# Kernel tuning notes

Measured on AMD Instinct MI355X. Metric: run time of the kernel, lower is better.

The kernel has to match this reference:

```python
import jax, jax.numpy as jnp
import numpy as np

EPS = 0.001
CTX = 8
POWERS = 2.0 ** jnp.arange(CTX - 1, -1, -1, dtype=jnp.float32)  # [2^7,...,1]


def _normalize_rows(x):
    return x / jnp.linalg.norm(x, axis=1, keepdims=True)


def _layer(side, inp, normal, offset, W, bias):
    # inp: None for first layer, else previous layer output
    if inp is None:
        inp = jnp.concatenate([bias, jax.nn.sigmoid(jnp.clip(side, EPS, 1.0 - EPS))])
    else:
        inp = jnp.concatenate([bias, inp])
    bits = (side @ normal > offset).astype(jnp.float32)          # [CTX]
    gating = jnp.dot(bits, POWERS).astype(jnp.int32)              # scalar context index
    logit_in = jnp.log(inp) - jnp.log1p(-inp)                     # torch.logit
    out = jax.nn.sigmoid(logit_in @ W[gating])                    # gather slice + GEMV
    return jnp.clip(out, EPS, 1.0 - EPS)


def setup_inputs() -> dict:
    key = jax.random.key(0)
    ks = jax.random.split(key, 10)
    input_dim, dims = 1024, [1024, 1024, 512, 1]  # [in] + layer_dims + [out]
    side_info = jax.random.normal(ks[0], (input_dim,), dtype=jnp.float32)
    d = {"side_info": side_info}
    for i, (p, c) in enumerate(zip(dims[:-1], dims[1:])):
        d[f"W{i}"] = jnp.full((2 ** CTX, p + 1, c), 1.0 / (p + 1), dtype=jnp.float32)
        d[f"N{i}"] = _normalize_rows(jax.random.normal(ks[1 + i], (input_dim, CTX), dtype=jnp.float32))
        d[f"O{i}"] = jax.random.normal(ks[4 + i], (CTX,), dtype=jnp.float32)
        d[f"B{i}"] = EPS + jax.random.uniform(ks[7 + i], (1,), dtype=jnp.float32) * (1.0 - 2.0 * EPS)
    return d


def reference(side_info, W0, W1, W2, N0, N1, N2, O0, O1, O2, B0, B1, B2):
    side = side_info.astype(jnp.float32)
    out = None
    for W, N, O, B in ((W0, N0, O0, B0), (W1, N1, O1, B1), (W2, N2, O2, B2)):
        out = _layer(side, out, N, O, W, B)
    return out
```

## Files before the change

### kernel.cpp

```cpp
#include <hip/hip_runtime.h>
#include <math.h>

#define GLN_EPS 0.001f

__device__ __forceinline__ float clipf_(float v) {
    return fminf(fmaxf(v, GLN_EPS), 1.0f - GLN_EPS);
}
__device__ __forceinline__ float logitf_(float p) {
    return logf(p) - log1pf(-p);
}
__device__ __forceinline__ float sigclip_logit(float z) {
    float s = 1.0f / (1.0f + expf(-z));
    s = clipf_(s);
    return logf(s) - log1pf(-s);
}


__global__ __launch_bounds__(256) void gln_prep(
    const float* __restrict__ side,
    const float* __restrict__ N0, const float* __restrict__ O0,
    const float* __restrict__ N1, const float* __restrict__ O1,
    const float* __restrict__ N2, const float* __restrict__ O2,
    float* __restrict__ ws)
{
    const int bid = blockIdx.x, tid = threadIdx.x;
    if (bid == 0) {
        for (int i = tid; i < 1536; i += 256) ws[i] = 0.0f;
        return;
    }
    const float* __restrict__ N = (bid == 1) ? N0 : (bid == 2) ? N1 : N2;
    const float* __restrict__ O = (bid == 1) ? O0 : (bid == 2) ? O1 : O2;

    float p[8];
#pragma unroll
    for (int k = 0; k < 8; ++k) p[k] = 0.0f;

    for (int i = tid; i < 1024; i += 256) {
        const float s = side[i];
        const float4* n4 = reinterpret_cast<const float4*>(N + (size_t)i * 8);
        const float4 a = n4[0];
        const float4 b = n4[1];
        p[0] += s * a.x; p[1] += s * a.y; p[2] += s * a.z; p[3] += s * a.w;
        p[4] += s * b.x; p[5] += s * b.y; p[6] += s * b.z; p[7] += s * b.w;
    }

    __shared__ float red[4][8];
    const int lane = tid & 63, wid = tid >> 6;
#pragma unroll
    for (int k = 0; k < 8; ++k) {
        float v = p[k];
#pragma unroll
        for (int off = 32; off > 0; off >>= 1) v += __shfl_down(v, off);
        if (lane == 0) red[wid][k] = v;
    }
    __syncthreads();
    if (tid == 0) {
        int g = 0;
#pragma unroll
        for (int k = 0; k < 8; ++k) {
            const float d = red[0][k] + red[1][k] + red[2][k] + red[3][k];
            if (d > O[k]) g |= 1 << (7 - k);
        }
        reinterpret_cast<int*>(ws)[1536 + (bid - 1)] = g;
    }
}

__global__ __launch_bounds__(256) void gln_gemv0(
    const float* __restrict__ side,
    const float* __restrict__ W0,
    const float* __restrict__ B0,
    float* __restrict__ ws)
{
    const int g = reinterpret_cast<const int*>(ws)[1536];
    const float lb = logitf_(B0[0]);
    const size_t base = (size_t)g * 1025u * 1024u;
    const int col = threadIdx.x * 4;

    float4 acc = make_float4(0.f, 0.f, 0.f, 0.f);
    for (int i = blockIdx.x; i < 1025; i += gridDim.x) {
        const float xi = (i == 0) ? lb : clipf_(side[i - 1]);
        const float4 w = *reinterpret_cast<const float4*>(W0 + base + (size_t)i * 1024u + col);
        acc.x += xi * w.x; acc.y += xi * w.y; acc.z += xi * w.z; acc.w += xi * w.w;
    }
    atomicAdd(&ws[col + 0], acc.x);
    atomicAdd(&ws[col + 1], acc.y);
    atomicAdd(&ws[col + 2], acc.z);
    atomicAdd(&ws[col + 3], acc.w);
}

__global__ __launch_bounds__(256) void gln_gemv1(
    const float* __restrict__ W1,
    const float* __restrict__ B1,
    float* __restrict__ ws)
{
    const int g = reinterpret_cast<const int*>(ws)[1537];
    const float lb = logitf_(B1[0]);
    const size_t base = (size_t)g * 1025u * 512u;
    const int col = threadIdx.x * 2;

    float2 acc = make_float2(0.f, 0.f);
    for (int i = blockIdx.x; i < 1025; i += gridDim.x) {
        const float xi = (i == 0) ? lb : sigclip_logit(ws[i - 1]);
        const float2 w = *reinterpret_cast<const float2*>(W1 + base + (size_t)i * 512u + col);
        acc.x += xi * w.x; acc.y += xi * w.y;
    }
    atomicAdd(&ws[1024 + col + 0], acc.x);
    atomicAdd(&ws[1024 + col + 1], acc.y);
}

__global__ __launch_bounds__(256) void gln_final(
    const float* __restrict__ W2,
    const float* __restrict__ B2,
    float* __restrict__ ws,
    float* __restrict__ out)
{
    const int g = reinterpret_cast<const int*>(ws)[1538];
    const size_t base = (size_t)g * 513u;
    const int tid = threadIdx.x;

    float partial = 0.0f;
    for (int i = tid; i < 513; i += 256) {
        const float xi = (i == 0) ? logitf_(B2[0]) : sigclip_logit(ws[1024 + i - 1]);
        partial += xi * W2[base + i];
    }

    __shared__ float red[4];
#pragma unroll
    for (int off = 32; off > 0; off >>= 1) partial += __shfl_down(partial, off);
    if ((tid & 63) == 0) red[tid >> 6] = partial;
    __syncthreads();
    if (tid == 0) {
        const float z = red[0] + red[1] + red[2] + red[3];
        float o = 1.0f / (1.0f + expf(-z));
        out[0] = clipf_(o);
    }
}

extern "C" void kernel_launch(void* const* d_in, const int* in_sizes, int n_in,
                              void* d_out, int out_size, void* d_ws, size_t ws_size,
                              hipStream_t stream) {
    const float* side = (const float*)d_in[0];
    const float* W0   = (const float*)d_in[1];
    const float* N0   = (const float*)d_in[2];
    const float* O0   = (const float*)d_in[3];
    const float* B0   = (const float*)d_in[4];
    const float* W1   = (const float*)d_in[5];
    const float* N1   = (const float*)d_in[6];
    const float* O1   = (const float*)d_in[7];
    const float* B1   = (const float*)d_in[8];
    const float* W2   = (const float*)d_in[9];
    const float* N2   = (const float*)d_in[10];
    const float* O2   = (const float*)d_in[11];
    const float* B2   = (const float*)d_in[12];
    float* out = (float*)d_out;
    float* ws  = (float*)d_ws;

    hipLaunchKernelGGL(gln_prep,  dim3(4),  dim3(256), 0, stream,
                       side, N0, O0, N1, O1, N2, O2, ws);
    hipLaunchKernelGGL(gln_gemv0, dim3(64), dim3(256), 0, stream, side, W0, B0, ws);
    hipLaunchKernelGGL(gln_gemv1, dim3(64), dim3(256), 0, stream, W1, B1, ws);
    hipLaunchKernelGGL(gln_final, dim3(1),  dim3(256), 0, stream, W2, B2, ws, out);
}
```

Before: 1.433 ms.

## Fuse all GLN stages into one cooperative kernel with grid syncs

Replaces four separate launches with one cooperative kernel of 256 blocks that uses grid-wide syncs between the gating, layer-0 GEMV, layer-1 GEMV and final dot-product stages. The GEMVs are re-tiled so each block covers a 64-column chunk and a strided set of rows, reducing partials in shared memory before one atomic per column. The layer-1 GEMV now uses float4 loads instead of float2. The aim is to remove launch gaps and to spread the 4 MB selected weight slice over many more blocks, since the old 64-block grid left much of the GPU idle. The cost is grid-sync overhead, and the cooperative launch requires all 256 blocks to be co-resident.

```diff
diff --git a/kernel.cpp b/kernel.cpp
--- a/kernel.cpp
+++ b/kernel.cpp
@@ -1,7 +1,11 @@
 #include <hip/hip_runtime.h>
+#include <hip/hip_cooperative_groups.h>
 #include <math.h>
 
+namespace cg = cooperative_groups;
+
 #define GLN_EPS 0.001f
+#define NBLK 256
 
 __device__ __forceinline__ float clipf_(float v) {
     return fminf(fmaxf(v, GLN_EPS), 1.0f - GLN_EPS);
@@ -15,149 +19,148 @@
     return logf(s) - log1pf(-s);
 }
 
+struct GlnArgs {
+    const float *side, *W0, *N0, *O0, *B0;
+    const float *W1, *N1, *O1, *B1;
+    const float *W2, *N2, *O2, *B2;
+    float* ws;
+    float* out;
+};
 
-__global__ __launch_bounds__(256) void gln_prep(
-    const float* __restrict__ side,
-    const float* __restrict__ N0, const float* __restrict__ O0,
-    const float* __restrict__ N1, const float* __restrict__ O1,
-    const float* __restrict__ N2, const float* __restrict__ O2,
-    float* __restrict__ ws)
+
+__global__ __launch_bounds__(256) void gln_fused(GlnArgs a)
 {
+    __shared__ float sred[16 * 64];
+    __shared__ float red8[4][8];
+
     const int bid = blockIdx.x, tid = threadIdx.x;
-    if (bid == 0) {
-        for (int i = tid; i < 1536; i += 256) ws[i] = 0.0f;
-        return;
-    }
-    const float* __restrict__ N = (bid == 1) ? N0 : (bid == 2) ? N1 : N2;
-    const float* __restrict__ O = (bid == 1) ? O0 : (bid == 2) ? O1 : O2;
+    float* ws = a.ws;
 
-    float p[8];
+    if (bid < 3) {
+        const float* __restrict__ N = (bid == 0) ? a.N0 : (bid == 1) ? a.N1 : a.N2;
+        const float* __restrict__ O = (bid == 0) ? a.O0 : (bid == 1) ? a.O1 : a.O2;
+        float p[8];
 #pragma unroll
-    for (int k = 0; k < 8; ++k) p[k] = 0.0f;
-
-    for (int i = tid; i < 1024; i += 256) {
-        const float s = side[i];
-        const float4* n4 = reinterpret_cast<const float4*>(N + (size_t)i * 8);
-        const float4 a = n4[0];
-        const float4 b = n4[1];
-        p[0] += s * a.x; p[1] += s * a.y; p[2] += s * a.z; p[3] += s * a.w;
-        p[4] += s * b.x; p[5] += s * b.y; p[6] += s * b.z; p[7] += s * b.w;
-    }
-
-    __shared__ float red[4][8];
-    const int lane = tid & 63, wid = tid >> 6;
-#pragma unroll
-    for (int k = 0; k < 8; ++k) {
-        float v = p[k];
-#pragma unroll
-        for (int off = 32; off > 0; off >>= 1) v += __shfl_down(v, off);
-        if (lane == 0) red[wid][k] = v;
-    }
-    __syncthreads();
-    if (tid == 0) {
-        int g = 0;
+        for (int k = 0; k < 8; ++k) p[k] = 0.0f;
+        for (int i = tid; i < 1024; i += 256) {
+            const float s = a.side[i];
+            const float4* n4 = reinterpret_cast<const float4*>(N + (size_t)i * 8);
+            const float4 u = n4[0], v = n4[1];
+            p[0] += s * u.x; p[1] += s * u.y; p[2] += s * u.z; p[3] += s * u.w;
+            p[4] += s * v.x; p[5] += s * v.y; p[6] += s * v.z; p[7] += s * v.w;
+        }
+        const int lane = tid & 63, wid = tid >> 6;
 #pragma unroll
         for (int k = 0; k < 8; ++k) {
-            const float d = red[0][k] + red[1][k] + red[2][k] + red[3][k];
-            if (d > O[k]) g |= 1 << (7 - k);
+            float v = p[k];
+#pragma unroll
+            for (int off = 32; off > 0; off >>= 1) v += __shfl_down(v, off);
+            if (lane == 0) red8[wid][k] = v;
         }
-        reinterpret_cast<int*>(ws)[1536 + (bid - 1)] = g;
+        __syncthreads();
+        if (tid == 0) {
+            int g = 0;
+#pragma unroll
+            for (int k = 0; k < 8; ++k) {
+                const float d = red8[0][k] + red8[1][k] + red8[2][k] + red8[3][k];
+                if (d > O[k]) g |= 1 << (7 - k);
+            }
+            reinterpret_cast<int*>(ws)[1536 + bid] = g;
+        }
+    } else if (bid == 3) {
+        for (int i = tid; i < 1536; i += 256) ws[i] = 0.0f;
     }
-}
+    cg::this_grid().sync();
 
-__global__ __launch_bounds__(256) void gln_gemv0(
-    const float* __restrict__ side,
-    const float* __restrict__ W0,
-    const float* __restrict__ B0,
-    float* __restrict__ ws)
-{
-    const int g = reinterpret_cast<const int*>(ws)[1536];
-    const float lb = logitf_(B0[0]);
-    const size_t base = (size_t)g * 1025u * 1024u;
-    const int col = threadIdx.x * 4;
+    {
+        const int g0 = reinterpret_cast<const int*>(ws)[1536];
+        const float lb = logitf_(a.B0[0]);
+        const size_t base = (size_t)g0 * (1025u * 1024u);
+        const int colchunk = bid & 15;
+        const int c16 = tid & 15, r16 = tid >> 4;
+        const int rowid = ((bid >> 4) << 4) | r16;
+        const int col = colchunk * 64 + c16 * 4;
 
-    float4 acc = make_float4(0.f, 0.f, 0.f, 0.f);
-    for (int i = blockIdx.x; i < 1025; i += gridDim.x) {
-        const float xi = (i == 0) ? lb : clipf_(side[i - 1]);
-        const float4 w = *reinterpret_cast<const float4*>(W0 + base + (size_t)i * 1024u + col);
-        acc.x += xi * w.x; acc.y += xi * w.y; acc.z += xi * w.z; acc.w += xi * w.w;
+        float4 acc = make_float4(0.f, 0.f, 0.f, 0.f);
+        for (int i = rowid; i < 1025; i += 256) {
+            const float xi = (i == 0) ? lb : clipf_(a.side[i - 1]);
+            const float4 w = *reinterpret_cast<const float4*>(a.W0 + base + (size_t)i * 1024u + col);
+            acc.x += xi * w.x; acc.y += xi * w.y; acc.z += xi * w.z; acc.w += xi * w.w;
+        }
+        *reinterpret_cast<float4*>(&sred[r16 * 64 + c16 * 4]) = acc;
+        __syncthreads();
+        if (tid < 64) {
+            float s = 0.0f;
+#pragma unroll
+            for (int r = 0; r < 16; ++r) s += sred[r * 64 + tid];
+            atomicAdd(&ws[colchunk * 64 + tid], s);
+        }
     }
-    atomicAdd(&ws[col + 0], acc.x);
-    atomicAdd(&ws[col + 1], acc.y);
-    atomicAdd(&ws[col + 2], acc.z);
-    atomicAdd(&ws[col + 3], acc.w);
-}
+    cg::this_grid().sync();
 
-__global__ __launch_bounds__(256) void gln_gemv1(
-    const float* __restrict__ W1,
-    const float* __restrict__ B1,
-    float* __restrict__ ws)
-{
-    const int g = reinterpret_cast<const int*>(ws)[1537];
-    const float lb = logitf_(B1[0]);
-    const size_t base = (size_t)g * 1025u * 512u;
-    const int col = threadIdx.x * 2;
+    {
+        const int g1 = reinterpret_cast<const int*>(ws)[1537];
+        const float lb = logitf_(a.B1[0]);
+        const size_t base = (size_t)g1 * (1025u * 512u);
+        const int colchunk = bid & 7;
+        const int c16 = tid & 15, r16 = tid >> 4;
+        const int rowid = ((bid >> 3) << 4) | r16;
+        const int col = colchunk * 64 + c16 * 4;
 
-    float2 acc = make_float2(0.f, 0.f);
-    for (int i = blockIdx.x; i < 1025; i += gridDim.x) {
-        const float xi = (i == 0) ? lb : sigclip_logit(ws[i - 1]);
-        const float2 w = *reinterpret_cast<const float2*>(W1 + base + (size_t)i * 512u + col);
-        acc.x += xi * w.x; acc.y += xi * w.y;
+        float4 acc = make_float4(0.f, 0.f, 0.f, 0.f);
+        for (int i = rowid; i < 1025; i += 512) {
+            const float xi = (i == 0) ? lb : sigclip_logit(ws[i - 1]);
+            const float4 w = *reinterpret_cast<const float4*>(a.W1 + base + (size_t)i * 512u + col);
+            acc.x += xi * w.x; acc.y += xi * w.y; acc.z += xi * w.z; acc.w += xi * w.w;
+        }
+        __syncthreads();
+        *reinterpret_cast<float4*>(&sred[r16 * 64 + c16 * 4]) = acc;
+        __syncthreads();
+        if (tid < 64) {
+            float s = 0.0f;
+#pragma unroll
+            for (int r = 0; r < 16; ++r) s += sred[r * 64 + tid];
+            atomicAdd(&ws[1024 + colchunk * 64 + tid], s);
+        }
     }
-    atomicAdd(&ws[1024 + col + 0], acc.x);
-    atomicAdd(&ws[1024 + col + 1], acc.y);
-}
+    cg::this_grid().sync();
 
-__global__ __launch_bounds__(256) void gln_final(
-    const float* __restrict__ W2,
-    const float* __restrict__ B2,
-    float* __restrict__ ws,
-    float* __restrict__ out)
-{
-    const int g = reinterpret_cast<const int*>(ws)[1538];
-    const size_t base = (size_t)g * 513u;
-    const int tid = threadIdx.x;
-
-    float partial = 0.0f;
-    for (int i = tid; i < 513; i += 256) {
-        const float xi = (i == 0) ? logitf_(B2[0]) : sigclip_logit(ws[1024 + i - 1]);
-        partial += xi * W2[base + i];
-    }
-
-    __shared__ float red[4];
+    if (bid == 0) {
+        const int g2 = reinterpret_cast<const int*>(ws)[1538];
+        const float lb = logitf_(a.B2[0]);
+        const size_t base = (size_t)g2 * 513u;
+        float partial = 0.0f;
+        for (int i = tid; i < 513; i += 256) {
+            const float xi = (i == 0) ? lb : sigclip_logit(ws[1024 + i - 1]);
+            partial += xi * a.W2[base + i];
+        }
 #pragma unroll
-    for (int off = 32; off > 0; off >>= 1) partial += __shfl_down(partial, off);
-    if ((tid & 63) == 0) red[tid >> 6] = partial;
-    __syncthreads();
-    if (tid == 0) {
-        const float z = red[0] + red[1] + red[2] + red[3];
-        float o = 1.0f / (1.0f + expf(-z));
-        out[0] = clipf_(o);
+        for (int off = 32; off > 0; off >>= 1) partial += __shfl_down(partial, off);
+        __syncthreads();
+        if ((tid & 63) == 0) red8[tid >> 6][0] = partial;
+        __syncthreads();
+        if (tid == 0) {
+            const float z = red8[0][0] + red8[1][0] + red8[2][0] + red8[3][0];
+            a.out[0] = clipf_(1.0f / (1.0f + expf(-z)));
+        }
     }
 }
 
 extern "C" void kernel_launch(void* const* d_in, const int* in_sizes, int n_in,
                               void* d_out, int out_size, void* d_ws, size_t ws_size,
                               hipStream_t stream) {
-    const float* side = (const float*)d_in[0];
-    const float* W0   = (const float*)d_in[1];
-    const float* N0   = (const float*)d_in[2];
-    const float* O0   = (const float*)d_in[3];
-    const float* B0   = (const float*)d_in[4];
-    const float* W1   = (const float*)d_in[5];
-    const float* N1   = (const float*)d_in[6];
-    const float* O1   = (const float*)d_in[7];
-    const float* B1   = (const float*)d_in[8];
-    const float* W2   = (const float*)d_in[9];
-    const float* N2   = (const float*)d_in[10];
-    const float* O2   = (const float*)d_in[11];
-    const float* B2   = (const float*)d_in[12];
-    float* out = (float*)d_out;
-    float* ws  = (float*)d_ws;
+    GlnArgs a;
+    a.side = (const float*)d_in[0];
+    a.W0 = (const float*)d_in[1];  a.N0 = (const float*)d_in[2];
+    a.O0 = (const float*)d_in[3];  a.B0 = (const float*)d_in[4];
+    a.W1 = (const float*)d_in[5];  a.N1 = (const float*)d_in[6];
+    a.O1 = (const float*)d_in[7];  a.B1 = (const float*)d_in[8];
+    a.W2 = (const float*)d_in[9];  a.N2 = (const float*)d_in[10];
+    a.O2 = (const float*)d_in[11]; a.B2 = (const float*)d_in[12];
+    a.ws  = (float*)d_ws;
+    a.out = (float*)d_out;
 
-    hipLaunchKernelGGL(gln_prep,  dim3(4),  dim3(256), 0, stream,
-                       side, N0, O0, N1, O1, N2, O2, ws);
-    hipLaunchKernelGGL(gln_gemv0, dim3(64), dim3(256), 0, stream, side, W0, B0, ws);
-    hipLaunchKernelGGL(gln_gemv1, dim3(64), dim3(256), 0, stream, W1, B1, ws);
-    hipLaunchKernelGGL(gln_final, dim3(1),  dim3(256), 0, stream, W2, B2, ws, out);
+    void* params[] = { &a };
+    hipLaunchCooperativeKernel(reinterpret_cast<void*>(gln_fused),
+                               dim3(NBLK), dim3(256), params, 0, stream);
 }
```

Result: slower. 1.500 ms (+4.7%).
